# Optimization experiments

Measured on AMD Instinct MI355X. Metric: run time of the kernel, lower is better.

The kernel has to match this reference:

```python
import jax, jax.numpy as jnp
import numpy as np

N_DIM, D_SKETCH, M_COLS = 8192, 1024, 4096


def setup_inputs() -> dict:
    key = jax.random.key(0)
    kM, kD, kP = jax.random.split(key, 3)
    M = jax.random.normal(kM, (N_DIM, M_COLS), dtype=jnp.float32)
    # Rademacher signs, exactly as 2*(rand > 0.5).float() - 1
    D = 2.0 * (jax.random.uniform(kD, (N_DIM,)) > 0.5).astype(jnp.float32) - 1.0
    # np.random.choice(N, d) samples with replacement -> plain randint
    P = jax.random.randint(kP, (D_SKETCH,), 0, N_DIM)
    return {"M": M, "D": D, "P": P}


def _idct_rows(X, rows):
    # torch_dct.idct with norm=None along the last axis, evaluated only at the
    # output positions `rows` (identical values to full idct followed by gather):
    #   x[n] = (1/N) * ( X[...,0]/2 + sum_{k=1}^{N-1} X[...,k] * cos(pi*(2n+1)*k/(2N)) )
    N = X.shape[-1]
    k = jnp.arange(N, dtype=jnp.float32)
    w = jnp.where(k == 0, 0.5, 1.0) / N                      # DCT-III weights / N
    n = rows.astype(jnp.float32)
    ang = (jnp.pi / (2.0 * N)) * (2.0 * n[:, None] + 1.0) * k[None, :]
    C = jnp.cos(ang) * w[None, :]                            # [d, N]
    return jnp.einsum('dk,mk->md', C, X)                     # [m, d]


def reference(M, D, P):
    # SRFT sketch, 2-D branch, transpose=False:
    #   result = idct((D[:, None] * M).T).T[P, :]   ->  shape [d, m]
    X = D[:, None] * M                                       # sign flip, [N, m]
    out = _idct_rows(X.T, P)                                 # [m, d]
    return out.T                                             # [d, m]
```

## Files before the change

### kernel.cpp

```cpp
#include <hip/hip_runtime.h>

#define K_DIM 8192
#define M_OUT 1024
#define N_OUT 4096
#define BUFSZ 65536

typedef __attribute__((ext_vector_type(4))) float f32x4;
typedef __attribute__((ext_vector_type(8))) __bf16 bf16x8;
typedef __attribute__((ext_vector_type(2))) __bf16 bf16x2;
typedef __attribute__((ext_vector_type(4))) unsigned u32x4;
typedef __attribute__((ext_vector_type(8))) unsigned short u16x8;

__device__ __forceinline__ unsigned short f2bf(float x) {
  unsigned u = __builtin_bit_cast(unsigned, x);
  u += 0x7fffu + ((u >> 16) & 1u);
  return (unsigned short)(u >> 16);
}

__device__ __forceinline__ unsigned pack2(float a, float b) {
  bf16x2 v;
  v[0] = (__bf16)a;
  v[1] = (__bf16)b;
  return __builtin_bit_cast(unsigned, v);
}

__global__ __launch_bounds__(256) void build_c_kernel(
    const int* __restrict__ Pp, const float* __restrict__ Dp,
    unsigned short* __restrict__ Cm) {
  const int p = blockIdx.x;
  const int n2 = 2 * Pp[p] + 1;
  const int t = threadIdx.x;
#pragma unroll
  for (int ch = 0; ch < 4; ++ch) {
    const int kb = (ch << 11) + (t << 3);
    u16x8 o;
#pragma unroll
    for (int i = 0; i < 8; ++i) {
      const int k = kb + i;
      const unsigned tt = ((unsigned)(n2 * k)) & 32767u;
      const float cv = cosf((float)tt * 1.9174759848570515e-4f);
      const float wk = (k == 0) ? (0.5f / 8192.0f) : (1.0f / 8192.0f);
      o[i] = f2bf(cv * wk * Dp[k]);
    }
    *(u16x8*)(Cm + ((size_t)p << 13) + kb) = o;
  }
}

__global__ __launch_bounds__(512, 1) void gemm_kernel(
    const unsigned short* __restrict__ Cm, const float* __restrict__ Mp,
    float* __restrict__ outp, int kchunk, int nwg) {
  __shared__ __align__(16) char lds[2 * BUFSZ];

  const int id = blockIdx.x;
  const int chunk = nwg >> 3;
  const int sid = (id & 7) * chunk + (id >> 3);
  const int bm = sid & 3, bn = (sid >> 2) & 15, bz = sid >> 6;

  const int t = threadIdx.x;
  const int w = t >> 6, l = t & 63;
  const int wr = w >> 2, wc = w & 3;
  const int lg = l >> 4, lr = l & 15;
  const int k_begin = bz * kchunk;
  const int NT = kchunk >> 6;

  const int arow = t >> 3;
  const int acol = ((t & 7) << 4) ^ ((arow & 7) << 4);
  const char* Agl = (const char*)Cm + ((size_t)(bm * 256 + arow) << 14) +
                    ((size_t)k_begin << 1) + acol;
  auto stageA = [&](int nbuf, int tile) {
    char* d = (char*)lds + nbuf * BUFSZ + t * 16;
    const char* s = Agl + ((size_t)tile << 7);
#pragma unroll
    for (int i = 0; i < 4; ++i)
      __builtin_amdgcn_global_load_lds(
          (const __attribute__((address_space(1))) void*)(s + ((size_t)i << 20)),
          (__attribute__((address_space(3))) void*)(d + i * 8192), 16, 0, 0);
  };

  const float* Bg = Mp + (size_t)k_begin * N_OUT + bn * 256 + l * 4;
  auto loadB = [&](f32x4 (&r)[8], int tile, int half) {
#pragma unroll
    for (int i = 0; i < 4; ++i)
      r[half * 4 + i] =
          *(const f32x4*)(Bg + (size_t)(tile * 64 + w * 8 + half * 4 + i) * N_OUT);
  };
  auto writeB = [&](const f32x4 (&r)[8], int nbuf, int nn) {
    const int n = (l << 2) + nn;
    const int sN = (n & 7) ^ ((n >> 2) & 7);
    u32x4 pk;
#pragma unroll
    for (int j = 0; j < 4; ++j) pk[j] = pack2(r[2 * j][nn], r[2 * j + 1][nn]);
    *(u32x4*)(lds + nbuf * BUFSZ + 32768 + n * 128 + ((w ^ sN) << 4)) = pk;
  };

  const int sw = (lr & 7) << 4;
  const int xk0 = (lg << 4) ^ sw;
  const int xk1 = (64 + (lg << 4)) ^ sw;
  unsigned boff[2][4];
#pragma unroll
  for (int kk = 0; kk < 2; ++kk)
#pragma unroll
    for (int nf = 0; nf < 4; ++nf) {
      const int row = wc * 64 + nf * 16 + lr;
      const int sN = (row & 7) ^ ((row >> 2) & 7);
      boff[kk][nf] = 32768 + row * 128 + ((((kk << 2) | lg) ^ sN) << 4);
    }

  f32x4 acc[8][4] = {};
  bf16x8 Af[4];
  bf16x8 Bf[4];

  auto readA = [&](const char* aBuf, int mh, int xk) {
#pragma unroll
    for (int m = 0; m < 4; ++m)
      Af[m] = *(const bf16x8*)(aBuf + mh * 8192 + m * 2048 + xk);
  };
  auto readB = [&](int nbuf, int kk) {
#pragma unroll
    for (int nf = 0; nf < 4; ++nf)
      Bf[nf] = *(const bf16x8*)(lds + nbuf * BUFSZ + boff[kk][nf]);
  };
  auto mm = [&](int mh) {
    __builtin_amdgcn_s_setprio(1);
#pragma unroll
    for (int m = 0; m < 4; ++m)
#pragma unroll
      for (int nf = 0; nf < 4; ++nf)
        acc[mh * 4 + m][nf] = __builtin_amdgcn_mfma_f32_16x16x32_bf16(
            Af[m], Bf[nf], acc[mh * 4 + m][nf], 0, 0, 0);
    __builtin_amdgcn_s_setprio(0);
  };

  {
    f32x4 p[8];
    stageA(0, 0);
    loadB(p, 0, 0);
    loadB(p, 0, 1);
#pragma unroll
    for (int nn = 0; nn < 4; ++nn) writeB(p, 0, nn);
    asm volatile("s_waitcnt vmcnt(0) lgkmcnt(0)" ::: "memory");
    __builtin_amdgcn_sched_barrier(0);
    __builtin_amdgcn_s_barrier();
  }

  for (int tt = 0; tt < NT; ++tt) {
    const int cur = tt & 1, nxt = cur ^ 1;
    const char* aBuf = (const char*)lds + cur * BUFSZ + wr * 16384 + lr * 128;
    const bool more = (tt + 1) < NT;
    f32x4 sb[8];
    if (more) {
      loadB(sb, tt + 1, 0);
      loadB(sb, tt + 1, 1);
      stageA(nxt, tt + 1);
    }
    readB(cur, 0);
    readA(aBuf, 0, xk0);
    mm(0);
    readA(aBuf, 1, xk0);
    mm(1);
    if (more) {
      writeB(sb, nxt, 0);
      writeB(sb, nxt, 1);
      writeB(sb, nxt, 2);
      writeB(sb, nxt, 3);
    }
    readB(cur, 1);
    readA(aBuf, 0, xk1);
    mm(0);
    readA(aBuf, 1, xk1);
    mm(1);
    asm volatile("s_waitcnt vmcnt(0) lgkmcnt(0)" ::: "memory");
    __builtin_amdgcn_sched_barrier(0);
    __builtin_amdgcn_s_barrier();
  }

  float* po = outp + (size_t)bz * (M_OUT * N_OUT);
  const int orow = bm * 256 + wr * 128;
  const int ocol = bn * 256 + wc * 64 + lr;
#pragma unroll
  for (int mi = 0; mi < 8; ++mi) {
    const int r0 = orow + (mi >> 2) * 64 + (mi & 3) * 16 + (lg << 2);
#pragma unroll
    for (int ni = 0; ni < 4; ++ni) {
      const int c = ocol + ni * 16;
#pragma unroll
      for (int q = 0; q < 4; ++q)
        po[(size_t)(r0 + q) * N_OUT + c] = acc[mi][ni][q];
    }
  }
}

__global__ __launch_bounds__(256) void reduce_kernel(
    const float* __restrict__ part, float* __restrict__ out, int ksplit) {
  const size_t total = (size_t)M_OUT * N_OUT;
  const size_t i = ((size_t)blockIdx.x * 256 + threadIdx.x) * 4;
  if (i >= total) return;
  f32x4 s = *(const f32x4*)(part + i);
  for (int s2 = 1; s2 < ksplit; ++s2) s += *(const f32x4*)(part + (size_t)s2 * total + i);
  *(f32x4*)(out + i) = s;
}

__global__ __launch_bounds__(256) void naive_kernel(
    const float* __restrict__ Mp, const float* __restrict__ Dp,
    const int* __restrict__ Pp, float* __restrict__ out) {
  const int p = blockIdx.y;
  const int j = blockIdx.x * 256 + threadIdx.x;
  const int n2 = 2 * Pp[p] + 1;
  float acc = 0.0f;
  for (int k = 0; k < K_DIM; ++k) {
    const unsigned tt = ((unsigned)(n2 * k)) & 32767u;
    const float cv = cosf((float)tt * 1.9174759848570515e-4f);
    const float wk = (k == 0) ? 0.5f : 1.0f;
    acc += cv * wk * Dp[k] * Mp[(size_t)k * N_OUT + j];
  }
  out[(size_t)p * N_OUT + j] = acc * (1.0f / 8192.0f);
}

extern "C" void kernel_launch(void* const* d_in, const int* in_sizes, int n_in,
                              void* d_out, int out_size, void* d_ws, size_t ws_size,
                              hipStream_t stream) {
  const float* Mp = (const float*)d_in[0];
  const float* Dp = (const float*)d_in[1];
  const int* Pp = (const int*)d_in[2];
  float* out = (float*)d_out;

  const size_t CM_BYTES = (size_t)M_OUT * K_DIM * 2;
  const size_t PART_BYTES = (size_t)M_OUT * N_OUT * 4;

  int ksplit;
  if (ws_size >= CM_BYTES + 4 * PART_BYTES) ksplit = 4;
  else if (ws_size >= CM_BYTES + 2 * PART_BYTES) ksplit = 2;
  else if (ws_size >= CM_BYTES) ksplit = 1;
  else ksplit = 0;

  if (ksplit == 0) {
    naive_kernel<<<dim3(N_OUT / 256, M_OUT), 256, 0, stream>>>(Mp, Dp, Pp, out);
    return;
  }

  unsigned short* Cm = (unsigned short*)d_ws;
  float* part = (float*)((char*)d_ws + CM_BYTES);

  build_c_kernel<<<dim3(M_OUT), 256, 0, stream>>>(Pp, Dp, Cm);

  float* gout = (ksplit > 1) ? part : out;
  const int kchunk = K_DIM / ksplit;
  const int nwg = 64 * ksplit;
  gemm_kernel<<<dim3(nwg), 512, 0, stream>>>(Cm, Mp, gout, kchunk, nwg);

  if (ksplit > 1)
    reduce_kernel<<<dim3((M_OUT * N_OUT / 4 + 255) / 256), 256, 0, stream>>>(part, out, ksplit);
}
```

Measured before the change: 109.0 us.

## Shrink GEMM tile to 256x128, use two waves per SIMD, and cut K-split to two

The GEMM tile changes from 256x256 to 256x128 and the wave layout from 2x4 to 4x2. This halves the accumulators per wave and cuts LDS to 96KB, so two workgroups can fit per CU. K-split drops from 4 to 2, which halves the partial-sum traffic written by the GEMM and read by the reduce kernel. The B global loads are now prefetched two tiles ahead in a register double buffer with partial vmcnt waits and extra barriers inside each tile. The trade-off is more A re-reads from global memory because tiles are narrower, and more barrier synchronisation per tile.

```diff
diff --git a/kernel.cpp b/kernel.cpp
--- a/kernel.cpp
+++ b/kernel.cpp
@@ -3,12 +3,11 @@
 #define K_DIM 8192
 #define M_OUT 1024
 #define N_OUT 4096
-#define BUFSZ 65536
+#define BUFSZ 49152
 
 typedef __attribute__((ext_vector_type(4))) float f32x4;
 typedef __attribute__((ext_vector_type(8))) __bf16 bf16x8;
 typedef __attribute__((ext_vector_type(2))) __bf16 bf16x2;
-typedef __attribute__((ext_vector_type(4))) unsigned u32x4;
 typedef __attribute__((ext_vector_type(8))) unsigned short u16x8;
 
 __device__ __forceinline__ unsigned short f2bf(float x) {
@@ -46,7 +45,7 @@
   }
 }
 
-__global__ __launch_bounds__(512, 1) void gemm_kernel(
+__global__ __launch_bounds__(512, 2) void gemm_kernel(
     const unsigned short* __restrict__ Cm, const float* __restrict__ Mp,
     float* __restrict__ outp, int kchunk, int nwg) {
   __shared__ __align__(16) char lds[2 * BUFSZ];
@@ -54,11 +53,11 @@
   const int id = blockIdx.x;
   const int chunk = nwg >> 3;
   const int sid = (id & 7) * chunk + (id >> 3);
-  const int bm = sid & 3, bn = (sid >> 2) & 15, bz = sid >> 6;
+  const int bz = sid & 1, bm = (sid >> 1) & 3, bn = sid >> 3;
 
   const int t = threadIdx.x;
   const int w = t >> 6, l = t & 63;
-  const int wr = w >> 2, wc = w & 3;
+  const int wr = w >> 1, wc = w & 1;
   const int lg = l >> 4, lr = l & 15;
   const int k_begin = bz * kchunk;
   const int NT = kchunk >> 6;
@@ -77,20 +76,25 @@
           (__attribute__((address_space(3))) void*)(d + i * 8192), 16, 0, 0);
   };
 
-  const float* Bg = Mp + (size_t)k_begin * N_OUT + bn * 256 + l * 4;
-  auto loadB = [&](f32x4 (&r)[8], int tile, int half) {
+  const int bk0 = w * 8 + (l >> 5) * 4;
+  const int bn0 = (l & 31) * 4;
+  const float* Bg = Mp + (size_t)k_begin * N_OUT + bn * 128 + bn0;
+  auto loadB = [&](f32x4 (&r)[4], int tile) {
 #pragma unroll
     for (int i = 0; i < 4; ++i)
-      r[half * 4 + i] =
-          *(const f32x4*)(Bg + (size_t)(tile * 64 + w * 8 + half * 4 + i) * N_OUT);
-  };
-  auto writeB = [&](const f32x4 (&r)[8], int nbuf, int nn) {
-    const int n = (l << 2) + nn;
-    const int sN = (n & 7) ^ ((n >> 2) & 7);
-    u32x4 pk;
-#pragma unroll
-    for (int j = 0; j < 4; ++j) pk[j] = pack2(r[2 * j][nn], r[2 * j + 1][nn]);
-    *(u32x4*)(lds + nbuf * BUFSZ + 32768 + n * 128 + ((w ^ sN) << 4)) = pk;
+      r[i] = *(const f32x4*)(Bg + (size_t)(tile * 64 + bk0 + i) * N_OUT);
+  };
+  auto writeB = [&](const f32x4 (&r)[4], int nbuf) {
+#pragma unroll
+    for (int nn = 0; nn < 4; ++nn) {
+      const int n = bn0 + nn;
+      const int sN = (n & 7) ^ ((n >> 2) & 7);
+      uint2 pk;
+      pk.x = pack2(r[0][nn], r[1][nn]);
+      pk.y = pack2(r[2][nn], r[3][nn]);
+      *(uint2*)(lds + nbuf * BUFSZ + 32768 + n * 128 + ((w ^ sN) << 4) +
+                ((l >> 5) << 3)) = pk;
+    }
   };
 
   const int sw = (lr & 7) << 4;
@@ -106,86 +110,85 @@
       boff[kk][nf] = 32768 + row * 128 + ((((kk << 2) | lg) ^ sN) << 4);
     }
 
-  f32x4 acc[8][4] = {};
+  f32x4 acc[4][4] = {};
   bf16x8 Af[4];
   bf16x8 Bf[4];
 
-  auto readA = [&](const char* aBuf, int mh, int xk) {
+  auto readA = [&](int nbuf, int xk) {
+    const char* aBuf = (const char*)lds + nbuf * BUFSZ + wr * 8192 + lr * 128;
 #pragma unroll
     for (int m = 0; m < 4; ++m)
-      Af[m] = *(const bf16x8*)(aBuf + mh * 8192 + m * 2048 + xk);
+      Af[m] = *(const bf16x8*)(aBuf + m * 2048 + xk);
   };
   auto readB = [&](int nbuf, int kk) {
 #pragma unroll
     for (int nf = 0; nf < 4; ++nf)
       Bf[nf] = *(const bf16x8*)(lds + nbuf * BUFSZ + boff[kk][nf]);
   };
-  auto mm = [&](int mh) {
+  auto mm = [&]() {
     __builtin_amdgcn_s_setprio(1);
 #pragma unroll
     for (int m = 0; m < 4; ++m)
 #pragma unroll
       for (int nf = 0; nf < 4; ++nf)
-        acc[mh * 4 + m][nf] = __builtin_amdgcn_mfma_f32_16x16x32_bf16(
-            Af[m], Bf[nf], acc[mh * 4 + m][nf], 0, 0, 0);
+        acc[m][nf] = __builtin_amdgcn_mfma_f32_16x16x32_bf16(
+            Af[m], Bf[nf], acc[m][nf], 0, 0, 0);
     __builtin_amdgcn_s_setprio(0);
   };
 
+  f32x4 sbA[4], sbB[4];
+
   {
-    f32x4 p[8];
     stageA(0, 0);
-    loadB(p, 0, 0);
-    loadB(p, 0, 1);
-#pragma unroll
-    for (int nn = 0; nn < 4; ++nn) writeB(p, 0, nn);
+    loadB(sbB, 1);
+    f32x4 p0[4];
+    loadB(p0, 0);
+    writeB(p0, 0);
     asm volatile("s_waitcnt vmcnt(0) lgkmcnt(0)" ::: "memory");
     __builtin_amdgcn_sched_barrier(0);
     __builtin_amdgcn_s_barrier();
   }
 
-  for (int tt = 0; tt < NT; ++tt) {
+  auto tile_body = [&](int tt, f32x4 (&sbLoad)[4], f32x4 (&sbWrite)[4]) {
     const int cur = tt & 1, nxt = cur ^ 1;
-    const char* aBuf = (const char*)lds + cur * BUFSZ + wr * 16384 + lr * 128;
-    const bool more = (tt + 1) < NT;
-    f32x4 sb[8];
-    if (more) {
-      loadB(sb, tt + 1, 0);
-      loadB(sb, tt + 1, 1);
-      stageA(nxt, tt + 1);
-    }
+    readA(cur, xk0);
     readB(cur, 0);
-    readA(aBuf, 0, xk0);
-    mm(0);
-    readA(aBuf, 1, xk0);
-    mm(1);
-    if (more) {
-      writeB(sb, nxt, 0);
-      writeB(sb, nxt, 1);
-      writeB(sb, nxt, 2);
-      writeB(sb, nxt, 3);
-    }
+    if (tt + 1 < NT) stageA(nxt, tt + 1);
+    if (tt + 2 < NT) loadB(sbLoad, tt + 2);
+    __builtin_amdgcn_s_barrier();
+    asm volatile("s_waitcnt lgkmcnt(0)" ::: "memory");
+    __builtin_amdgcn_sched_barrier(0);
+    mm();
+    __builtin_amdgcn_s_barrier();
+    readA(cur, xk1);
     readB(cur, 1);
-    readA(aBuf, 0, xk1);
-    mm(0);
-    readA(aBuf, 1, xk1);
-    mm(1);
-    asm volatile("s_waitcnt vmcnt(0) lgkmcnt(0)" ::: "memory");
-    __builtin_amdgcn_sched_barrier(0);
-    __builtin_amdgcn_s_barrier();
+    if (tt + 1 < NT) writeB(sbWrite, nxt);
+    asm volatile("s_waitcnt lgkmcnt(0)" ::: "memory");
+    __builtin_amdgcn_sched_barrier(0);
+    mm();
+    if (tt + 2 < NT) { asm volatile("s_waitcnt vmcnt(4)" ::: "memory"); }
+    else             { asm volatile("s_waitcnt vmcnt(0)" ::: "memory"); }
+    __builtin_amdgcn_sched_barrier(0);
+    __builtin_amdgcn_s_barrier();
+  };
+
+  for (int tt = 0; tt < NT; tt += 2) {
+    tile_body(tt, sbA, sbB);
+    tile_body(tt + 1, sbB, sbA);
   }
 
   float* po = outp + (size_t)bz * (M_OUT * N_OUT);
-  const int orow = bm * 256 + wr * 128;
-  const int ocol = bn * 256 + wc * 64 + lr;
-#pragma unroll
-  for (int mi = 0; mi < 8; ++mi) {
-    const int r0 = orow + (mi >> 2) * 64 + (mi & 3) * 16 + (lg << 2);
-#pragma unroll
-    for (int ni = 0; ni < 4; ++ni) {
-      const int c = ocol + ni * 16;
+  const int orow = bm * 256 + wr * 64;
+  const int ocol = bn * 128 + wc * 64 + lr;
+#pragma unroll
+  for (int m = 0; m < 4; ++m) {
+    const int r0 = orow + m * 16 + (lg << 2);
+#pragma unroll
+    for (int nf = 0; nf < 4; ++nf) {
+      const int c = ocol + nf * 16;
 #pragma unroll
       for (int q = 0; q < 4; ++q)
-        po[(size_t)(r0 + q) * N_OUT + c] = acc[mi][ni][q];
+        po[(size_t)(r0 + q) * N_OUT + c] = acc[m][nf][q];
     }
   }
 }
@@ -228,8 +231,7 @@
   const size_t PART_BYTES = (size_t)M_OUT * N_OUT * 4;
 
   int ksplit;
-  if (ws_size >= CM_BYTES + 4 * PART_BYTES) ksplit = 4;
-  else if (ws_size >= CM_BYTES + 2 * PART_BYTES) ksplit = 2;
+  if (ws_size >= CM_BYTES + 2 * PART_BYTES) ksplit = 2;
   else if (ws_size >= CM_BYTES) ksplit = 1;
   else ksplit = 0;
 
@@ -245,7 +247,7 @@
 
   float* gout = (ksplit > 1) ? part : out;
   const int kchunk = K_DIM / ksplit;
-  const int nwg = 64 * ksplit;
+  const int nwg = (M_OUT / 256) * (N_OUT / 128) * ksplit;
   gemm_kernel<<<dim3(nwg), 512, 0, stream>>>(Cm, Mp, gout, kchunk, nwg);
 
   if (ksplit > 1)
```

New measurement: 123.4 us. 1.13x slower.
